# Optimization experiments

Hardware: AMD Instinct MI355X
Metric: run time of the kernel (lower is better)

The kernel has to match this reference:

```python
import jax, jax.numpy as jnp
import numpy as np

HEADS = 8
EPS = 1e-5


def layernorm(x, g, b):
    mu = jnp.mean(x, axis=-1, keepdims=True)
    var = jnp.mean((x - mu) ** 2, axis=-1, keepdims=True)
    return (x - mu) * jax.lax.rsqrt(var + EPS) * g + b


def setup_inputs() -> dict:
    key = jax.random.key(0)
    ks = jax.random.split(key, 5)
    B, C, H, W = 8, 384, 32, 32
    d = C
    s = 0.02
    return {
        "x": jax.random.normal(ks[0], (B, C, H, W), jnp.float32),
        "ln1_g": jnp.ones((d,), jnp.float32),
        "ln1_b": jnp.zeros((d,), jnp.float32),
        "lna_g": jnp.ones((d,), jnp.float32),
        "lna_b": jnp.zeros((d,), jnp.float32),
        "w_qkv": jax.random.normal(ks[1], (d, 3 * d), jnp.float32) * s,
        "w_out": jax.random.normal(ks[2], (d, d), jnp.float32) * s,
        "ln2_g": jnp.ones((d,), jnp.float32),
        "ln2_b": jnp.zeros((d,), jnp.float32),
        "w1": jax.random.normal(ks[3], (d, 4 * d), jnp.float32) * s,
        "b1": jnp.zeros((4 * d,), jnp.float32),
        "w2": jax.random.normal(ks[4], (4 * d, d), jnp.float32) * s,
        "b2": jnp.zeros((d,), jnp.float32),
    }


def reference(x, ln1_g, ln1_b, lna_g, lna_b, w_qkv, w_out, ln2_g, ln2_b, w1, b1, w2, b2):
    B, C, H, W = x.shape
    d = C
    dh = d // HEADS
    scale = dh ** (-0.5)
    # flatten spatial -> tokens: [B, N, C]
    t = x.reshape(B, C, H * W).transpose(0, 2, 1)

    # --- attention branch (note: double pre-norm, as in original) ---
    a = layernorm(t, ln1_g, ln1_b)
    a = layernorm(a, lna_g, lna_b)
    qkv = a @ w_qkv  # [B, N, 3d]
    q, k, v = jnp.split(qkv, 3, axis=-1)
    q = q.reshape(B, -1, HEADS, dh).transpose(0, 2, 1, 3)  # b h n d
    k = k.reshape(B, -1, HEADS, dh).transpose(0, 2, 1, 3)
    v = v.reshape(B, -1, HEADS, dh).transpose(0, 2, 1, 3)
    dots = jnp.einsum("bhnd,bhmd->bhnm", q, k) * scale
    attn = jax.nn.softmax(dots, axis=-1)
    o = jnp.einsum("bhnm,bhmd->bhnd", attn, v)
    o = o.transpose(0, 2, 1, 3).reshape(B, -1, d)
    t = t + o @ w_out

    # --- MLP branch (exact GELU, as torch nn.GELU default) ---
    m = layernorm(t, ln2_g, ln2_b)
    m = jax.nn.gelu(m @ w1 + b1, approximate=False) @ w2 + b2
    t = t + m

    return t.transpose(0, 2, 1).reshape(B, C, H, W)
```

## Files before the change

kernel.cpp:

```cpp
#include <hip/hip_runtime.h>
#include <math.h>

#define NTOK 1024
#define DM   384
#define NHEAD 8
#define DH   48
#define BATCH 8
#define NROWS (BATCH * NTOK)
#define SC2   (0.14433756729740643f * 1.4426950408889634f)

typedef __attribute__((ext_vector_type(8))) _Float16 f16x8;
typedef __attribute__((ext_vector_type(2))) __fp16 fp16x2_raw;
typedef __attribute__((ext_vector_type(4))) float f32x4;

#define ASYNC16(gp, lp) __builtin_amdgcn_global_load_lds( \
    (const __attribute__((address_space(1))) void*)(gp),  \
    (__attribute__((address_space(3))) void*)(lp), 16, 0, 0)

#define EXP2R(x) __builtin_amdgcn_exp2f(x)
#define RCPR(x)  __builtin_amdgcn_rcpf(x)

__device__ __forceinline__ unsigned int pkh(float a, float b) {
    union { fp16x2_raw h; unsigned int u; } cv;
    cv.h = __builtin_amdgcn_cvt_pkrtz(a, b);
    return cv.u;
}

__device__ __forceinline__ float gelu_fast(float v) {
    const float u = v * (0.7978845608f + 0.0356774081f * v * v);
    const float e = EXP2R(fminf(u * 2.885390082f, 120.0f));
    return v * e * RCPR(e + 1.0f);
}

__global__ __launch_bounds__(256) void prep_kernel(const float* __restrict__ x,
                                                   const float* __restrict__ ln1_g,
                                                   const float* __restrict__ ln1_b,
                                                   const float* __restrict__ lna_g,
                                                   const float* __restrict__ lna_b,
                                                   float* __restrict__ t,
                                                   _Float16* __restrict__ a_h,
                                                   const float* __restrict__ wqkv,
                                                   const float* __restrict__ wout,
                                                   const float* __restrict__ w1,
                                                   const float* __restrict__ w2,
                                                   _Float16* __restrict__ wqkvT,
                                                   _Float16* __restrict__ woutT,
                                                   _Float16* __restrict__ w1T,
                                                   _Float16* __restrict__ w2T) {
    __shared__ float Ts[32][389];
    const int bid = blockIdx.x;
    const int tid = threadIdx.x;

    if (bid >= 256) {
        float (*tile)[33] = (float(*)[33])&Ts[0][0];
        const int wb = bid - 256;
        const float* W; _Float16* Wt; int K, N, nx, tt;
        if (wb < 432)       { W = wqkv; Wt = wqkvT; K = 384;  N = 1152; nx = 36; tt = wb; }
        else if (wb < 576)  { W = wout; Wt = woutT; K = 384;  N = 384;  nx = 12; tt = wb - 432; }
        else if (wb < 1152) { W = w1;   Wt = w1T;   K = 384;  N = 1536; nx = 48; tt = wb - 576; }
        else                { W = w2;   Wt = w2T;   K = 1536; N = 384;  nx = 12; tt = wb - 1152; }
        const int n0 = (tt % nx) * 32, k0 = (tt / nx) * 32;
        const int tx = tid & 31, ty = tid >> 5;
        #pragma unroll
        for (int i = ty; i < 32; i += 8)
            tile[i][tx] = W[(size_t)(k0 + i) * N + n0 + tx];
        __syncthreads();
        #pragma unroll
        for (int i = ty; i < 32; i += 8)
            Wt[(size_t)(n0 + i) * K + k0 + tx] = (_Float16)tile[tx][i];
        return;
    }

    const int b = bid >> 5, n0 = (bid & 31) * 32;
    const int tx = tid & 31, ty8 = tid >> 5;
    const float* xb = x + (size_t)b * (DM * NTOK);
    #pragma unroll
    for (int c0 = 0; c0 < DM; c0 += 32) {
        #pragma unroll
        for (int i = ty8; i < 32; i += 8)
            Ts[tx][c0 + i] = xb[(size_t)(c0 + i) * NTOK + n0 + tx];
    }
    __syncthreads();

    const int g = tid >> 3, sub = tid & 7;
    const int c0 = sub * 48;
    float xv[48];
    #pragma unroll
    for (int k = 0; k < 12; ++k)
        *(float4*)&xv[k * 4] = *(const float4*)&Ts[g][c0 + k * 4];

    const size_t trow = (size_t)((b << 10) + n0 + g) * DM;
    float s = 0.0f, sq = 0.0f;
    #pragma unroll
    for (int k = 0; k < 12; ++k)
        *(float4*)&t[trow + c0 + k * 4] = *(const float4*)&xv[k * 4];
    #pragma unroll
    for (int j = 0; j < 48; ++j) { s += xv[j]; sq += xv[j] * xv[j]; }
    s += __shfl_xor(s, 1, 64); sq += __shfl_xor(sq, 1, 64);
    s += __shfl_xor(s, 2, 64); sq += __shfl_xor(sq, 2, 64);
    s += __shfl_xor(s, 4, 64); sq += __shfl_xor(sq, 4, 64);
    float mu = s * (1.0f / DM);
    float var = fmaxf(sq * (1.0f / DM) - mu * mu, 0.0f);
    float r1 = rsqrtf(var + 1e-5f);

    float s2 = 0.0f, q2 = 0.0f;
    #pragma unroll
    for (int k = 0; k < 12; ++k) {
        const float4 gk = *(const float4*)&ln1_g[c0 + k * 4];
        const float4 bk = *(const float4*)&ln1_b[c0 + k * 4];
        float y0 = (xv[k*4+0] - mu) * r1 * gk.x + bk.x;
        float y1 = (xv[k*4+1] - mu) * r1 * gk.y + bk.y;
        float y2 = (xv[k*4+2] - mu) * r1 * gk.z + bk.z;
        float y3 = (xv[k*4+3] - mu) * r1 * gk.w + bk.w;
        xv[k*4+0] = y0; xv[k*4+1] = y1; xv[k*4+2] = y2; xv[k*4+3] = y3;
        s2 += (y0 + y1) + (y2 + y3);
        q2 += (y0*y0 + y1*y1) + (y2*y2 + y3*y3);
    }
    s2 += __shfl_xor(s2, 1, 64); q2 += __shfl_xor(q2, 1, 64);
    s2 += __shfl_xor(s2, 2, 64); q2 += __shfl_xor(q2, 2, 64);
    s2 += __shfl_xor(s2, 4, 64); q2 += __shfl_xor(q2, 4, 64);
    mu = s2 * (1.0f / DM);
    var = fmaxf(q2 * (1.0f / DM) - mu * mu, 0.0f);
    const float r2 = rsqrtf(var + 1e-5f);

    unsigned int d[12];
    #pragma unroll
    for (int k = 0; k < 12; ++k) {
        const float4 gk = *(const float4*)&lna_g[c0 + k * 4];
        const float4 bk = *(const float4*)&lna_b[c0 + k * 4];
        const float y0 = (xv[k*4+0] - mu) * r2 * gk.x + bk.x;
        const float y1 = (xv[k*4+1] - mu) * r2 * gk.y + bk.y;
        const float y2 = (xv[k*4+2] - mu) * r2 * gk.z + bk.z;
        const float y3 = (xv[k*4+3] - mu) * r2 * gk.w + bk.w;
        d[k*2+0] = pkh(y0, y1); d[k*2+1] = pkh(y2, y3);
    }
    unsigned int* op = (unsigned int*)(a_h + trow + c0);
    #pragma unroll
    for (int k = 0; k < 3; ++k)
        *(uint4*)(op + k * 4) = *(const uint4*)&d[k * 4];
}

template <int EPI, int BN>
__global__ __launch_bounds__(256) void gemm_f16(const _Float16* __restrict__ A,
                                                const _Float16* __restrict__ Bt,
                                                const float* __restrict__ bias,
                                                const float* __restrict__ R,
                                                _Float16* __restrict__ Ch,
                                                float* __restrict__ Cf,
                                                int M, int N, int K) {
    constexpr int NFRAG = BN / 32;
    __shared__ _Float16 As[128][64];
    __shared__ _Float16 Bs[BN][64];
    const int tid = threadIdx.x;
    const int w = tid >> 6, lane = tid & 63;
    const int l15 = lane & 15, lq = lane >> 4;
    const int bm = blockIdx.y * 128, bn = blockIdx.x * BN;
    const int moff = (w & 1) * 64, noff = (w >> 1) * (BN / 2);

    const int srw = lane >> 3, pp = lane & 7;
    const int c = pp ^ srw;
    const _Float16* Ag[4];
    const _Float16* Bg[BN / 32];
    #pragma unroll
    for (int j = 0; j < 4; ++j)
        Ag[j] = A + (size_t)(bm + w * 32 + j * 8 + srw) * K + c * 8;
    #pragma unroll
    for (int j = 0; j < BN / 32; ++j)
        Bg[j] = Bt + (size_t)(bn + w * (BN / 4) + j * 8 + srw) * K + c * 8;

    const int octA = ((lq ^ (l15 & 7)) << 4);

    f32x4 acc[4][NFRAG];
    #pragma unroll
    for (int mi = 0; mi < 4; ++mi)
        #pragma unroll
        for (int ni = 0; ni < NFRAG; ++ni) acc[mi][ni] = (f32x4){0.f, 0.f, 0.f, 0.f};

    for (int k0 = 0; k0 < K; k0 += 64) {
        __syncthreads();
        #pragma unroll
        for (int j = 0; j < 4; ++j) {
            ASYNC16(Ag[j], &As[w * 32 + j * 8][0]);
            Ag[j] += 64;
        }
        #pragma unroll
        for (int j = 0; j < BN / 32; ++j) {
            ASYNC16(Bg[j], &Bs[w * (BN / 4) + j * 8][0]);
            Bg[j] += 64;
        }
        __syncthreads();
        #pragma unroll
        for (int ks = 0; ks < 2; ++ks) {
            const int ox = octA ^ (ks << 6);
            f16x8 af[4], bfr[NFRAG];
            #pragma unroll
            for (int mi = 0; mi < 4; ++mi)
                af[mi] = *(const f16x8*)((const char*)As + ((moff + mi * 16 + l15) << 7) + ox);
            #pragma unroll
            for (int ni = 0; ni < NFRAG; ++ni)
                bfr[ni] = *(const f16x8*)((const char*)Bs + ((noff + ni * 16 + l15) << 7) + ox);
            #pragma unroll
            for (int mi = 0; mi < 4; ++mi)
                #pragma unroll
                for (int ni = 0; ni < NFRAG; ++ni)
                    acc[mi][ni] = __builtin_amdgcn_mfma_f32_16x16x32_f16(af[mi], bfr[ni], acc[mi][ni], 0, 0, 0);
        }
    }

    #pragma unroll
    for (int mi = 0; mi < 4; ++mi) {
        #pragma unroll
        for (int ni = 0; ni < NFRAG; ++ni) {
            const int col = bn + noff + ni * 16 + l15;
            float bv = 0.0f;
            if (EPI >= 2) bv = bias[col];
            if (EPI == 4) {
                const int row0 = bm + moff + mi * 16 + lq * 4;
                const int b = row0 >> 10, nn = row0 & 1023;
                float4 vv;
                vv.x = acc[mi][ni][0] + bv + R[(size_t)(row0 + 0) * N + col];
                vv.y = acc[mi][ni][1] + bv + R[(size_t)(row0 + 1) * N + col];
                vv.z = acc[mi][ni][2] + bv + R[(size_t)(row0 + 2) * N + col];
                vv.w = acc[mi][ni][3] + bv + R[(size_t)(row0 + 3) * N + col];
                *(float4*)(Cf + (size_t)b * (DM * NTOK) + (size_t)col * NTOK + nn) = vv;
            } else {
                #pragma unroll
                for (int r = 0; r < 4; ++r) {
                    const int row = bm + moff + mi * 16 + lq * 4 + r;
                    const size_t idx = (size_t)row * N + col;
                    float v = acc[mi][ni][r];
                    if (EPI == 2) v = gelu_fast(v + bv);
                    Ch[idx] = (_Float16)v;
                }
            }
        }
    }
}

__global__ __launch_bounds__(256) void gemm_out_ln(const _Float16* __restrict__ A,
                                                   const _Float16* __restrict__ Bt,
                                                   float* __restrict__ T,
                                                   _Float16* __restrict__ a_out,
                                                   const float* __restrict__ gg,
                                                   const float* __restrict__ bb) {
    __shared__ _Float16 As[2][32][64];
    __shared__ _Float16 Bs[2][384][64];
    __shared__ float red_s[4][16];
    __shared__ float red_q[4][16];
    const int tid = threadIdx.x;
    const int w = tid >> 6, lane = tid & 63;
    const int l15 = lane & 15, lq = lane >> 4;
    const int bm = blockIdx.x * 32;
    const int mr = (w & 1) * 16;
    const int cq = (w >> 1) * 192;

    const int srw = lane >> 3, pp = lane & 7;
    const int c = pp ^ srw;
    const _Float16* Ag = A + (size_t)(bm + w * 8 + srw) * 384 + c * 8;
    const _Float16* Bg[12];
    #pragma unroll
    for (int j = 0; j < 12; ++j)
        Bg[j] = Bt + (size_t)(j * 32 + w * 8 + srw) * 384 + c * 8;

    const int octA = ((lq ^ (l15 & 7)) << 4);

    f32x4 acc[12];
    #pragma unroll
    for (int ni = 0; ni < 12; ++ni) acc[ni] = (f32x4){0.f, 0.f, 0.f, 0.f};

    ASYNC16(Ag, &As[0][w * 8][0]); Ag += 64;
    #pragma unroll
    for (int j = 0; j < 12; ++j) { ASYNC16(Bg[j], &Bs[0][j * 32 + w * 8][0]); Bg[j] += 64; }

    for (int kt = 0; kt < 6; ++kt) {
        const int cur = kt & 1;
        __syncthreads();
        if (kt < 5) {
            ASYNC16(Ag, &As[cur ^ 1][w * 8][0]); Ag += 64;
            #pragma unroll
            for (int j = 0; j < 12; ++j) { ASYNC16(Bg[j], &Bs[cur ^ 1][j * 32 + w * 8][0]); Bg[j] += 64; }
        }
        #pragma unroll
        for (int ks = 0; ks < 2; ++ks) {
            const int ox = octA ^ (ks << 6);
            const f16x8 af = *(const f16x8*)((const char*)&As[cur][0][0] + ((mr + l15) << 7) + ox);
            #pragma unroll
            for (int ni = 0; ni < 12; ++ni) {
                const f16x8 bf = *(const f16x8*)((const char*)&Bs[cur][0][0] + ((cq + ni * 16 + l15) << 7) + ox);
                acc[ni] = __builtin_amdgcn_mfma_f32_16x16x32_f16(af, bf, acc[ni], 0, 0, 0);
            }
        }
    }

    float vv[12][4];
    float s[4] = {0.f, 0.f, 0.f, 0.f}, q[4] = {0.f, 0.f, 0.f, 0.f};
    #pragma unroll
    for (int ni = 0; ni < 12; ++ni) {
        const int col = cq + ni * 16 + l15;
        #pragma unroll
        for (int r = 0; r < 4; ++r) {
            const int row = bm + mr + lq * 4 + r;
            const float v = acc[ni][r] + T[(size_t)row * DM + col];
            vv[ni][r] = v;
            T[(size_t)row * DM + col] = v;
            s[r] += v; q[r] += v * v;
        }
    }
    #pragma unroll
    for (int off = 1; off < 16; off <<= 1) {
        #pragma unroll
        for (int r = 0; r < 4; ++r) {
            s[r] += __shfl_xor(s[r], off, 64);
            q[r] += __shfl_xor(q[r], off, 64);
        }
    }
    if (l15 == 0) {
        #pragma unroll
        for (int r = 0; r < 4; ++r) {
            red_s[w][lq * 4 + r] = s[r];
            red_q[w][lq * 4 + r] = q[r];
        }
    }
    __syncthreads();
    float mu[4], rs[4];
    #pragma unroll
    for (int r = 0; r < 4; ++r) {
        const float ts = s[r] + red_s[w ^ 2][lq * 4 + r];
        const float tq = q[r] + red_q[w ^ 2][lq * 4 + r];
        mu[r] = ts * (1.0f / DM);
        const float var = fmaxf(tq * (1.0f / DM) - mu[r] * mu[r], 0.0f);
        rs[r] = rsqrtf(var + 1e-5f);
    }
    #pragma unroll
    for (int ni = 0; ni < 12; ++ni) {
        const int col = cq + ni * 16 + l15;
        const float gv = gg[col], bv = bb[col];
        #pragma unroll
        for (int r = 0; r < 4; ++r) {
            const int row = bm + mr + lq * 4 + r;
            a_out[(size_t)row * DM + col] = (_Float16)((vv[ni][r] - mu[r]) * rs[r] * gv + bv);
        }
    }
}

__global__ __launch_bounds__(256) void attn_kernel(const _Float16* __restrict__ qkv,
                                                   _Float16* __restrict__ o) {
    __shared__ _Float16 Ks[2][64][64];
    __shared__ _Float16 Vt[2][48][72];
    __shared__ _Float16 Ps[4][16][72];
    const int tid = threadIdx.x;
    const int w = tid >> 6, lane = tid & 63;
    const int l15 = lane & 15, lq = lane >> 4;
    const int bid = blockIdx.x;
    const int bh = ((bid >> 3) & 7) * 8 + (bid & 7);
    const int qt0 = (bid >> 6) * 64;
    const int h = bh & 7, b = bh >> 3;

    const _Float16* qbase = qkv + (size_t)b * NTOK * 1152 + h * 48;
    const _Float16* kbase = qbase + 384;
    const _Float16* vbase = qbase + 768;

    f16x8 qf[2];
    {
        const size_t qrow = (size_t)(qt0 + w * 16 + l15) * 1152;
        qf[0] = *(const f16x8*)(qbase + qrow + lq * 8);
        if (lq < 2) qf[1] = *(const f16x8*)(qbase + qrow + 32 + lq * 8);
        else        qf[1] = (f16x8){(_Float16)0, (_Float16)0, (_Float16)0, (_Float16)0,
                                    (_Float16)0, (_Float16)0, (_Float16)0, (_Float16)0};
    }

    const int srw = lane >> 3, pp = lane & 7;
    const int ck = pp ^ srw;
    const int ckoff = (ck < 6) ? ck * 8 : (ck - 6) * 8;
    const _Float16* Kg = kbase + (size_t)(w * 16 + srw) * 1152 + ckoff;
    const int vtp = tid & 31, vfo = tid >> 5;
    const _Float16* Vg = vbase + (size_t)(vtp * 2) * 1152 + vfo * 8;

    const int octK = ((lq ^ (l15 & 7)) << 4);

    ASYNC16(Kg, &Ks[0][w * 16][0]);
    ASYNC16(Kg + 8 * 1152, &Ks[0][w * 16 + 8][0]);
    Kg += 64 * 1152;
    uint4 va, vb;
    if (vfo < 6) { va = *(const uint4*)Vg; vb = *(const uint4*)(Vg + 1152); }
    Vg += 64 * 1152;

    f32x4 oacc[3];
    float lpart = 0.0f;
    #pragma unroll
    for (int vf = 0; vf < 3; ++vf) oacc[vf] = (f32x4){0.f, 0.f, 0.f, 0.f};

    int cur = 0;
    for (int kt = 0; kt < 16; ++kt) {
        if (vfo < 6) {
            const unsigned short* as = (const unsigned short*)&va;
            const unsigned short* bs = (const unsigned short*)&vb;
            #pragma unroll
            for (int j = 0; j < 8; ++j) {
                const unsigned int dw = (unsigned int)as[j] | ((unsigned int)bs[j] << 16);
                *(unsigned int*)((char*)&Vt[cur][0][0] + (vfo * 8 + j) * 144 + vtp * 4) = dw;
            }
        }
        __syncthreads();
        if (kt < 15) {
            ASYNC16(Kg, &Ks[cur ^ 1][w * 16][0]);
            ASYNC16(Kg + 8 * 1152, &Ks[cur ^ 1][w * 16 + 8][0]);
            Kg += 64 * 1152;
            if (vfo < 6) { va = *(const uint4*)Vg; vb = *(const uint4*)(Vg + 1152); }
            Vg += 64 * 1152;
        }

        f32x4 sacc[4];
        #pragma unroll
        for (int mi = 0; mi < 4; ++mi) sacc[mi] = (f32x4){0.f, 0.f, 0.f, 0.f};
        #pragma unroll
        for (int ks = 0; ks < 2; ++ks) {
            const int ox = octK ^ (ks << 6);
            #pragma unroll
            for (int mi = 0; mi < 4; ++mi) {
                const f16x8 kf = *(const f16x8*)((const char*)&Ks[cur][0][0] + ((mi * 16 + l15) << 7) + ox);
                sacc[mi] = __builtin_amdgcn_mfma_f32_16x16x32_f16(kf, qf[ks], sacc[mi], 0, 0, 0);
            }
        }

        #pragma unroll
        for (int mi = 0; mi < 4; ++mi) {
            const float p0 = EXP2R(sacc[mi][0] * SC2);
            const float p1 = EXP2R(sacc[mi][1] * SC2);
            const float p2 = EXP2R(sacc[mi][2] * SC2);
            const float p3 = EXP2R(sacc[mi][3] * SC2);
            lpart += (p0 + p1) + (p2 + p3);
            uint2 d;
            d.x = pkh(p0, p1); d.y = pkh(p2, p3);
            *(uint2*)((char*)&Ps[w][0][0] + l15 * 144 + (mi * 16 + lq * 4) * 2) = d;
        }
        asm volatile("s_waitcnt lgkmcnt(0)" ::: "memory");

        #pragma unroll
        for (int ks = 0; ks < 2; ++ks) {
            const int kk2 = ks * 64 + lq * 16;
            const f16x8 pf = *(const f16x8*)((const char*)&Ps[w][0][0] + l15 * 144 + kk2);
            #pragma unroll
            for (int vf = 0; vf < 3; ++vf) {
                const f16x8 vv = *(const f16x8*)((const char*)&Vt[cur][0][0] + (vf * 16 + l15) * 144 + kk2);
                oacc[vf] = __builtin_amdgcn_mfma_f32_16x16x32_f16(vv, pf, oacc[vf], 0, 0, 0);
            }
        }
        cur ^= 1;
    }

    lpart += __shfl_xor(lpart, 16, 64);
    lpart += __shfl_xor(lpart, 32, 64);
    const float linv = RCPR(lpart);
    _Float16* ob = o + (size_t)(b * NTOK + qt0 + w * 16 + l15) * DM + h * DH;
    #pragma unroll
    for (int vf = 0; vf < 3; ++vf) {
        uint2 d;
        d.x = pkh(oacc[vf][0] * linv, oacc[vf][1] * linv);
        d.y = pkh(oacc[vf][2] * linv, oacc[vf][3] * linv);
        *(uint2*)(ob + vf * 16 + lq * 4) = d;
    }
}

extern "C" void kernel_launch(void* const* d_in, const int* in_sizes, int n_in,
                              void* d_out, int out_size, void* d_ws, size_t ws_size,
                              hipStream_t stream) {
    const float* x     = (const float*)d_in[0];
    const float* ln1_g = (const float*)d_in[1];
    const float* ln1_b = (const float*)d_in[2];
    const float* lna_g = (const float*)d_in[3];
    const float* lna_b = (const float*)d_in[4];
    const float* w_qkv = (const float*)d_in[5];
    const float* w_out = (const float*)d_in[6];
    const float* ln2_g = (const float*)d_in[7];
    const float* ln2_b = (const float*)d_in[8];
    const float* w1    = (const float*)d_in[9];
    const float* b1    = (const float*)d_in[10];
    const float* w2    = (const float*)d_in[11];
    const float* b2    = (const float*)d_in[12];
    float* out = (float*)d_out;

    char* wsb = (char*)d_ws;
    float* t          = (float*)(wsb);
    _Float16* a_h     = (_Float16*)(wsb + 12582912);
    _Float16* qkv_h   = (_Float16*)(wsb + 18874368);
    _Float16* o_h     = (_Float16*)(wsb + 37748736);
    _Float16* h1_h    = (_Float16*)(wsb + 44040192);
    _Float16* wqkvT   = (_Float16*)(wsb + 69206016);
    _Float16* woutT   = (_Float16*)(wsb + 70090752);
    _Float16* w1T     = (_Float16*)(wsb + 70385664);
    _Float16* w2T     = (_Float16*)(wsb + 71565312);

    prep_kernel<<<256 + 1728, 256, 0, stream>>>(x, ln1_g, ln1_b, lna_g, lna_b, t, a_h,
                                                w_qkv, w_out, w1, w2, wqkvT, woutT, w1T, w2T);
    gemm_f16<0, 128><<<dim3(9, 64), 256, 0, stream>>>(a_h, wqkvT, nullptr, nullptr, qkv_h, nullptr, NROWS, 3 * DM, DM);
    attn_kernel<<<1024, 256, 0, stream>>>(qkv_h, o_h);
    gemm_out_ln<<<256, 256, 0, stream>>>(o_h, woutT, t, a_h, ln2_g, ln2_b);
    gemm_f16<2, 128><<<dim3(12, 64), 256, 0, stream>>>(a_h, w1T, b1, nullptr, h1_h, nullptr, NROWS, 4 * DM, DM);
    gemm_f16<4, 64><<<dim3(6, 64), 256, 0, stream>>>(h1_h, w2T, b2, t, nullptr, out, NROWS, DM, 4 * DM);
}
```

Baseline: 225.4 us.

## Double-buffer LDS tiles in f16 GEMM and widen N tile to 192

The shared GEMM kernel now keeps two LDS buffers for the A and B tiles. It prefetches the next K-tile with async global-to-LDS loads while the MFMAs run on the current tile, so each iteration needs one barrier instead of two. The QKV and MLP-up GEMMs also switch to a 192-wide N tile with a smaller grid, and the launch bound asks for two blocks per CU. This targets exposed global-load latency and barrier cost, at the price of double the LDS use, fewer blocks for those launches, and the chance that the compiler adds conservative waits that undo the overlap.

```diff
diff --git a/kernel.cpp b/kernel.cpp
--- a/kernel.cpp
+++ b/kernel.cpp
@@ -141,16 +141,16 @@
 }
 
 template <int EPI, int BN>
-__global__ __launch_bounds__(256) void gemm_f16(const _Float16* __restrict__ A,
-                                                const _Float16* __restrict__ Bt,
-                                                const float* __restrict__ bias,
-                                                const float* __restrict__ R,
-                                                _Float16* __restrict__ Ch,
-                                                float* __restrict__ Cf,
-                                                int M, int N, int K) {
+__global__ __launch_bounds__(256, 2) void gemm_f16(const _Float16* __restrict__ A,
+                                                   const _Float16* __restrict__ Bt,
+                                                   const float* __restrict__ bias,
+                                                   const float* __restrict__ R,
+                                                   _Float16* __restrict__ Ch,
+                                                   float* __restrict__ Cf,
+                                                   int M, int N, int K) {
     constexpr int NFRAG = BN / 32;
-    __shared__ _Float16 As[128][64];
-    __shared__ _Float16 Bs[BN][64];
+    __shared__ _Float16 As[2][128][64];
+    __shared__ _Float16 Bs[2][BN][64];
     const int tid = threadIdx.x;
     const int w = tid >> 6, lane = tid & 63;
     const int l15 = lane & 15, lq = lane >> 4;
@@ -160,12 +160,12 @@
     const int srw = lane >> 3, pp = lane & 7;
     const int c = pp ^ srw;
     const _Float16* Ag[4];
-    const _Float16* Bg[BN / 32];
+    const _Float16* Bg[NFRAG];
     #pragma unroll
     for (int j = 0; j < 4; ++j)
         Ag[j] = A + (size_t)(bm + w * 32 + j * 8 + srw) * K + c * 8;
     #pragma unroll
-    for (int j = 0; j < BN / 32; ++j)
+    for (int j = 0; j < NFRAG; ++j)
         Bg[j] = Bt + (size_t)(bn + w * (BN / 4) + j * 8 + srw) * K + c * 8;
 
     const int octA = ((lq ^ (l15 & 7)) << 4);
@@ -176,29 +176,33 @@
         #pragma unroll
         for (int ni = 0; ni < NFRAG; ++ni) acc[mi][ni] = (f32x4){0.f, 0.f, 0.f, 0.f};
 
-    for (int k0 = 0; k0 < K; k0 += 64) {
+    #pragma unroll
+    for (int j = 0; j < 4; ++j) { ASYNC16(Ag[j], &As[0][w * 32 + j * 8][0]); Ag[j] += 64; }
+    #pragma unroll
+    for (int j = 0; j < NFRAG; ++j) { ASYNC16(Bg[j], &Bs[0][w * (BN / 4) + j * 8][0]); Bg[j] += 64; }
+
+    const int nkt = K >> 6;
+    for (int kt = 0; kt < nkt; ++kt) {
+        const int cur = kt & 1;
         __syncthreads();
-        #pragma unroll
-        for (int j = 0; j < 4; ++j) {
-            ASYNC16(Ag[j], &As[w * 32 + j * 8][0]);
-            Ag[j] += 64;
-        }
-        #pragma unroll
-        for (int j = 0; j < BN / 32; ++j) {
-            ASYNC16(Bg[j], &Bs[w * (BN / 4) + j * 8][0]);
-            Bg[j] += 64;
-        }
-        __syncthreads();
+        if (kt < nkt - 1) {
+            #pragma unroll
+            for (int j = 0; j < 4; ++j) { ASYNC16(Ag[j], &As[cur ^ 1][w * 32 + j * 8][0]); Ag[j] += 64; }
+            #pragma unroll
+            for (int j = 0; j < NFRAG; ++j) { ASYNC16(Bg[j], &Bs[cur ^ 1][w * (BN / 4) + j * 8][0]); Bg[j] += 64; }
+        }
+        const char* Ab = (const char*)&As[cur][0][0];
+        const char* Bb = (const char*)&Bs[cur][0][0];
         #pragma unroll
         for (int ks = 0; ks < 2; ++ks) {
             const int ox = octA ^ (ks << 6);
             f16x8 af[4], bfr[NFRAG];
             #pragma unroll
             for (int mi = 0; mi < 4; ++mi)
-                af[mi] = *(const f16x8*)((const char*)As + ((moff + mi * 16 + l15) << 7) + ox);
+                af[mi] = *(const f16x8*)(Ab + ((moff + mi * 16 + l15) << 7) + ox);
             #pragma unroll
             for (int ni = 0; ni < NFRAG; ++ni)
-                bfr[ni] = *(const f16x8*)((const char*)Bs + ((noff + ni * 16 + l15) << 7) + ox);
+                bfr[ni] = *(const f16x8*)(Bb + ((noff + ni * 16 + l15) << 7) + ox);
             #pragma unroll
             for (int mi = 0; mi < 4; ++mi)
                 #pragma unroll
@@ -493,9 +497,9 @@
 
     prep_kernel<<<256 + 1728, 256, 0, stream>>>(x, ln1_g, ln1_b, lna_g, lna_b, t, a_h,
                                                 w_qkv, w_out, w1, w2, wqkvT, woutT, w1T, w2T);
-    gemm_f16<0, 128><<<dim3(9, 64), 256, 0, stream>>>(a_h, wqkvT, nullptr, nullptr, qkv_h, nullptr, NROWS, 3 * DM, DM);
+    gemm_f16<0, 192><<<dim3(6, 64), 256, 0, stream>>>(a_h, wqkvT, nullptr, nullptr, qkv_h, nullptr, NROWS, 3 * DM, DM);
     attn_kernel<<<1024, 256, 0, stream>>>(qkv_h, o_h);
     gemm_out_ln<<<256, 256, 0, stream>>>(o_h, woutT, t, a_h, ln2_g, ln2_b);
-    gemm_f16<2, 128><<<dim3(12, 64), 256, 0, stream>>>(a_h, w1T, b1, nullptr, h1_h, nullptr, NROWS, 4 * DM, DM);
+    gemm_f16<2, 192><<<dim3(8, 64), 256, 0, stream>>>(a_h, w1T, b1, nullptr, h1_h, nullptr, NROWS, 4 * DM, DM);
     gemm_f16<4, 64><<<dim3(6, 64), 256, 0, stream>>>(h1_h, w2T, b2, t, nullptr, out, NROWS, DM, 4 * DM);
 }
```

New measurement: 219.3 us. 2.7% less time.
